# Kernel tuning notes

Measured on AMD Instinct MI355X. Metric: run time of the kernel, lower is better.

The kernel has to match this reference:

```python
import jax, jax.numpy as jnp
import numpy as np

H, D, BD = 4, 128, 128   # num_heads, head_dim, bias_dim
QDIM = KDIM = 64
VDIM = 1
N = 512
EPS = 1e-5

def mish(x):
    return x * jnp.tanh(jax.nn.softplus(x))

def layernorm(x, g, b):
    m = jnp.mean(x, axis=-1, keepdims=True)
    v = jnp.var(x, axis=-1, keepdims=True)
    return (x - m) * jax.lax.rsqrt(v + EPS) * g + b

def _xavier(k, shape):
    fan_out, fan_in = shape
    lim = np.sqrt(6.0 / (fan_in + fan_out)).astype(np.float32)
    return jax.random.uniform(k, shape, jnp.float32, -lim, lim)

def setup_inputs() -> dict:
    key = jax.random.key(0)
    ks = jax.random.split(key, 12)
    return {
        "q": jax.random.normal(ks[0], (N, QDIM), jnp.float32),
        "k": jax.random.normal(ks[1], (N, KDIM), jnp.float32),
        "v": jax.random.normal(ks[2], (N, VDIM), jnp.float32),
        "bias": jax.random.uniform(ks[3], (N, N, BD), jnp.float32),
        "Wq": _xavier(ks[4], (H * D, QDIM)), "bq": jnp.zeros((H * D,), jnp.float32),
        "Wk": _xavier(ks[5], (H * D, KDIM)), "bk": jnp.zeros((H * D,), jnp.float32),
        "Wqo": _xavier(ks[6], (QDIM, H * D)), "bqo": jnp.zeros((QDIM,), jnp.float32),
        "Wko": _xavier(ks[7], (KDIM, H * D)), "bko": jnp.zeros((KDIM,), jnp.float32),
        "q_ln_g": jnp.ones((QDIM,), jnp.float32), "q_ln_b": jnp.zeros((QDIM,), jnp.float32),
        "k_ln_g": jnp.ones((KDIM,), jnp.float32), "k_ln_b": jnp.zeros((KDIM,), jnp.float32),
        "Wb": _xavier(ks[8], (H * BD, BD)), "bb_": jnp.zeros((H * BD,), jnp.float32),
        "Wbo": _xavier(ks[9], (BD, H * BD)), "bbo": jnp.zeros((BD,), jnp.float32),
    }

def reference(q, k, v, bias, Wq, bq, Wk, bk, Wqo, bqo, Wko, bko,
              q_ln_g, q_ln_b, k_ln_g, k_ln_b, Wb, bb_, Wbo, bbo):
    Nq, Nk = q.shape[0], k.shape[0]
    # q/k projections -> [N, H, D]
    pq = (q @ Wq.T + bq).reshape(Nq, H, D)
    pk = (k @ Wk.T + bk).reshape(Nk, H, D)
    # distance bias: Linear(BD -> H*BD), per-head L2 norm -> [H, Nq, Nk]
    bias_p = bias @ Wb.T + bb_                                  # [Nq, Nk, H*BD]
    diffs = jnp.linalg.norm(bias_p.reshape(Nq, Nk, H, BD), axis=-1)  # [Nq, Nk, H]
    diffs = jnp.transpose(diffs, (2, 0, 1))                     # [H, Nq, Nk]
    # scaled dot product attention with additive distance bias
    logits = jnp.einsum('qhd,khd->hqk', pq, pk) / np.sqrt(D).astype(np.float32) + diffs
    attn = jax.nn.softmax(logits, axis=-1)                      # [H, Nq, Nk]
    vals = jnp.einsum('hqk,kv->hqv', attn, v)                   # v shared across heads
    # values.permute(1,0,2).reshape(Nq, vdim*H) then mean over last dim
    vals_mean = jnp.mean(jnp.transpose(vals, (1, 0, 2)).reshape(Nq, H * VDIM),
                         axis=-1, keepdims=True)                # [Nq, 1]
    # torch does proj.permute(1,2,0).reshape(N, H*D): (d, h)-major flattening
    pq_flat = jnp.transpose(pq, (0, 2, 1)).reshape(Nq, D * H)
    pk_flat = jnp.transpose(pk, (0, 2, 1)).reshape(Nk, D * H)
    q_new = layernorm(q + mish(pq_flat @ Wqo.T + bqo), q_ln_g, q_ln_b)
    k_new = layernorm(k + mish(pk_flat @ Wko.T + bko), k_ln_g, k_ln_b)
    bias_out = mish(bias_p @ Wbo.T + bbo)                       # [Nq, Nk, BD]
    return (q_new, k_new, vals_mean, bias_out)
```

## Files before the change

### kernel.cpp

```cpp
#include <hip/hip_runtime.h>

#define NN 512
#define MROWS (NN*NN)
#define LDK 136

typedef __attribute__((ext_vector_type(8))) short short8;
typedef __attribute__((ext_vector_type(16))) float floatx16;

__device__ __forceinline__ unsigned short f2bf(float f) {
    union { float f; unsigned u; } x; x.f = f;
    unsigned r = x.u + 0x7fffu + ((x.u >> 16) & 1u);
    return (unsigned short)(r >> 16);
}

__device__ __forceinline__ floatx16 zero16() {
    floatx16 z;
    #pragma unroll
    for (int i = 0; i < 16; ++i) z[i] = 0.f;
    return z;
}

__global__ __launch_bounds__(256) void pre_kernel(
    const float* __restrict__ q, const float* __restrict__ k,
    const float* __restrict__ Wq, const float* __restrict__ bq,
    const float* __restrict__ Wk, const float* __restrict__ bk,
    float* __restrict__ pq, float* __restrict__ pk,
    const float* __restrict__ Wb, const float* __restrict__ Wbo,
    unsigned short* __restrict__ wbf)
{
    int b = blockIdx.x;
    int tid = threadIdx.x;
    if (b >= 1024) {
        int i = (b - 1024) * 256 + tid;
        float v = (i < 65536) ? Wb[i] : Wbo[i - 65536];
        wbf[i] = f2bf(v);
        return;
    }
    __shared__ float xs[64];
    int n = b & 511;
    int is_k = b >> 9;
    const float* x  = is_k ? k  : q;
    const float* W  = is_k ? Wk : Wq;
    const float* bi = is_k ? bk : bq;
    float* out      = is_k ? pk : pq;
    if (tid < 16)
        reinterpret_cast<float4*>(xs)[tid] = reinterpret_cast<const float4*>(x + n*64)[tid];
    __syncthreads();
    #pragma unroll
    for (int jj = 0; jj < 2; ++jj) {
        int j = jj*256 + tid;
        const float4* wr = reinterpret_cast<const float4*>(W + j*64);
        float acc = bi[j];
        #pragma unroll
        for (int c = 0; c < 16; ++c) {
            float4 w4 = wr[c];
            float4 x4 = reinterpret_cast<const float4*>(xs)[c];
            acc += x4.x*w4.x + x4.y*w4.y + x4.z*w4.z + x4.w*w4.w;
        }
        out[n*512 + j] = acc;
    }
}

__global__ __launch_bounds__(256, 4) void bias_kernel(
    const float* __restrict__ bias, const unsigned short* __restrict__ wb_bf,
    const float* __restrict__ bb, const unsigned short* __restrict__ wbo_bf,
    const float* __restrict__ bbo, float* __restrict__ bias_out,
    float* __restrict__ diffs)
{
    __shared__ __align__(16) char smem[34816 + 256];
    unsigned short* lA = (unsigned short*)smem;
    unsigned short* lP = (unsigned short*)(smem + 17408);
    float* sq = (float*)(smem + 34816);
    float* lT = (float*)smem;

    const int tid = threadIdx.x;
    const int w   = tid >> 6;
    const int l   = tid & 63;
    const int l31 = l & 31;
    const int qh  = l >> 5;
    const long row0 = (long)blockIdx.x * 64;

    {
        const float* src = bias + row0 * 128;
        #pragma unroll
        for (int i = 0; i < 4; ++i) {
            int flat = i*2048 + tid*8;
            int r = flat >> 7, c = flat & 127;
            float4 v0 = *reinterpret_cast<const float4*>(src + flat);
            float4 v1 = *reinterpret_cast<const float4*>(src + flat + 4);
            ushort4 o0 = { f2bf(v0.x), f2bf(v0.y), f2bf(v0.z), f2bf(v0.w) };
            ushort4 o1 = { f2bf(v1.x), f2bf(v1.y), f2bf(v1.z), f2bf(v1.w) };
            *reinterpret_cast<ushort4*>(&lA[r*LDK + c])     = o0;
            *reinterpret_cast<ushort4*>(&lA[r*LDK + c + 4]) = o1;
        }
        if (tid < 64) sq[tid] = 0.f;
    }

    floatx16 acc2[2];
    acc2[0] = zero16(); acc2[1] = zero16();

    const unsigned short* wbbase  = wb_bf  + (w*32 + l31)*128 + qh*8;
    const unsigned short* wbobase = wbo_bf + (w*32 + l31)*512 + qh*8;

    __syncthreads();

    for (int h = 0; h < 4; ++h) {
        floatx16 acc1[2];
        acc1[0] = zero16(); acc1[1] = zero16();
        const unsigned short* wa = wbbase + h*16384;
        #pragma unroll
        for (int kk = 0; kk < 8; ++kk) {
            short8 afr = *reinterpret_cast<const short8*>(wa + kk*16);
            short8 b0  = *reinterpret_cast<const short8*>(&lA[(l31)*LDK      + kk*16 + qh*8]);
            short8 b1  = *reinterpret_cast<const short8*>(&lA[(32 + l31)*LDK + kk*16 + qh*8]);
            acc1[0] = __builtin_amdgcn_mfma_f32_32x32x16_bf16(afr, b0, acc1[0], 0, 0, 0);
            acc1[1] = __builtin_amdgcn_mfma_f32_32x32x16_bf16(afr, b1, acc1[1], 0, 0, 0);
        }

        float4 bbq[4];
        #pragma unroll
        for (int s = 0; s < 4; ++s)
            bbq[s] = *reinterpret_cast<const float4*>(bb + h*128 + w*32 + qh*4 + s*8);

        float ssum[2];
        ushort4 pk4[2][4];
        #pragma unroll
        for (int nt = 0; nt < 2; ++nt) {
            float sa = 0.f;
            #pragma unroll
            for (int s = 0; s < 4; ++s) {
                const float* bbp = (const float*)&bbq[s];
                float v0 = acc1[nt][s*4+0] + bbp[0];
                float v1 = acc1[nt][s*4+1] + bbp[1];
                float v2 = acc1[nt][s*4+2] + bbp[2];
                float v3 = acc1[nt][s*4+3] + bbp[3];
                sa += v0*v0 + v1*v1 + v2*v2 + v3*v3;
                pk4[nt][s] = (ushort4){ f2bf(v0), f2bf(v1), f2bf(v2), f2bf(v3) };
            }
            sa += __shfl_xor(sa, 32);
            ssum[nt] = sa;
        }

        __syncthreads();

        #pragma unroll
        for (int nt = 0; nt < 2; ++nt) {
            int m = nt*32 + l31;
            #pragma unroll
            for (int s = 0; s < 4; ++s)
                *reinterpret_cast<ushort4*>(&lP[m*LDK + w*32 + qh*4 + s*8]) = pk4[nt][s];
            if (l < 32) atomicAdd(&sq[m], ssum[nt]);
        }

        __syncthreads();

        if (tid < 64) {
            float s2 = sq[tid];
            diffs[(long)h*MROWS + row0 + tid] = sqrtf(s2);
            sq[tid] = 0.f;
        }

        const unsigned short* wo = wbobase + h*128;
        #pragma unroll
        for (int kk = 0; kk < 8; ++kk) {
            short8 afr = *reinterpret_cast<const short8*>(wo + kk*16);
            short8 b0  = *reinterpret_cast<const short8*>(&lP[(l31)*LDK      + kk*16 + qh*8]);
            short8 b1  = *reinterpret_cast<const short8*>(&lP[(32 + l31)*LDK + kk*16 + qh*8]);
            acc2[0] = __builtin_amdgcn_mfma_f32_32x32x16_bf16(afr, b0, acc2[0], 0, 0, 0);
            acc2[1] = __builtin_amdgcn_mfma_f32_32x32x16_bf16(afr, b1, acc2[1], 0, 0, 0);
        }
    }

    float4 bboq[4];
    #pragma unroll
    for (int s = 0; s < 4; ++s)
        bboq[s] = *reinterpret_cast<const float4*>(bbo + w*32 + qh*4 + s*8);

    float outs[2][16];
    #pragma unroll
    for (int nt = 0; nt < 2; ++nt) {
        #pragma unroll
        for (int s = 0; s < 4; ++s) {
            const float* bp = (const float*)&bboq[s];
            #pragma unroll
            for (int r = 0; r < 4; ++r) {
                float x = acc2[nt][s*4+r] + bp[r];
                float e = __expf(x);
                float u = 1.f + e, u2 = u*u;
                outs[nt][s*4+r] = (x > 15.f) ? x : x * (u2 - 1.f) / (u2 + 1.f);
            }
        }
    }

    __syncthreads();
    #pragma unroll
    for (int nt = 0; nt < 2; ++nt) {
        int m = nt*32 + l31;
        #pragma unroll
        for (int s = 0; s < 4; ++s)
            #pragma unroll
            for (int r = 0; r < 4; ++r)
                lT[m*LDK + w*32 + qh*4 + s*8 + r] = outs[nt][s*4+r];
    }
    __syncthreads();
    #pragma unroll
    for (int i = 0; i < 8; ++i) {
        int flat = i*1024 + tid*4;
        int r = flat >> 7, c = flat & 127;
        *reinterpret_cast<float4*>(bias_out + (row0 + r)*128 + c) =
            *reinterpret_cast<const float4*>(&lT[r*LDK + c]);
    }
}

__global__ __launch_bounds__(256) void qk_kernel(
    const float* __restrict__ pq, const float* __restrict__ pk,
    float* __restrict__ logits)
{
    __shared__ float A[64*128];
    __shared__ float BT[128*64];
    int blk = blockIdx.x;
    int kt = blk & 7, h = (blk >> 3) & 3, qt = blk >> 5;
    int tid = threadIdx.x;

    #pragma unroll
    for (int i = 0; i < 8; ++i) {
        int flat = i*1024 + tid*4;
        int r = flat >> 7, c = flat & 127;
        *reinterpret_cast<float4*>(&A[flat]) =
            *reinterpret_cast<const float4*>(pq + (size_t)(qt*64 + r)*512 + h*128 + c);
    }
    {
        int kk = tid & 63, g = tid >> 6;
        #pragma unroll
        for (int i = 0; i < 8; ++i) {
            int d0 = g*32 + i*4;
            float4 vv = *reinterpret_cast<const float4*>(pk + (size_t)(kt*64 + kk)*512 + h*128 + d0);
            BT[(d0+0)*64 + kk] = vv.x;
            BT[(d0+1)*64 + kk] = vv.y;
            BT[(d0+2)*64 + kk] = vv.z;
            BT[(d0+3)*64 + kk] = vv.w;
        }
    }
    __syncthreads();

    int qg = tid >> 4, kg = tid & 15;
    int qs = qg*4, ks = kg*4;
    float acc[4][4] = {};
    for (int d = 0; d < 128; d += 4) {
        float a_[4][4], b_[4][4];
        #pragma unroll
        for (int i = 0; i < 4; ++i) {
            float4 av = *reinterpret_cast<const float4*>(&A[(qs+i)*128 + d]);
            a_[i][0] = av.x; a_[i][1] = av.y; a_[i][2] = av.z; a_[i][3] = av.w;
        }
        #pragma unroll
        for (int dd = 0; dd < 4; ++dd) {
            float4 bv = *reinterpret_cast<const float4*>(&BT[(d+dd)*64 + ks]);
            b_[dd][0] = bv.x; b_[dd][1] = bv.y; b_[dd][2] = bv.z; b_[dd][3] = bv.w;
        }
        #pragma unroll
        for (int i = 0; i < 4; ++i)
            #pragma unroll
            for (int j = 0; j < 4; ++j)
                acc[i][j] += a_[i][0]*b_[0][j] + a_[i][1]*b_[1][j]
                           + a_[i][2]*b_[2][j] + a_[i][3]*b_[3][j];
    }

    const float scale = 0.088388347648318447f;
    #pragma unroll
    for (int i = 0; i < 4; ++i) {
        size_t off = (size_t)h*MROWS + (size_t)(qt*64 + qs + i)*512 + kt*64 + ks;
        float4* p = reinterpret_cast<float4*>(logits + off);
        float4 dv = *p;
        dv.x = fmaf(acc[i][0], scale, dv.x);
        dv.y = fmaf(acc[i][1], scale, dv.y);
        dv.z = fmaf(acc[i][2], scale, dv.z);
        dv.w = fmaf(acc[i][3], scale, dv.w);
        *p = dv;
    }
}

__global__ __launch_bounds__(256) void attnval_kernel(
    const float* __restrict__ logits, const float* __restrict__ v,
    float* __restrict__ vmean)
{
    __shared__ float red[32];
    int qrow = blockIdx.x, tid = threadIdx.x;
    int wid = tid >> 6;
    float vsum = 0.f;
    float v0 = v[tid], v1 = v[tid + 256];
    for (int h = 0; h < 4; ++h) {
        const float* lr = logits + (size_t)h*MROWS + (size_t)qrow*512;
        float l0 = lr[tid], l1 = lr[tid + 256];
        float m = fmaxf(l0, l1);
        #pragma unroll
        for (int o = 1; o < 64; o <<= 1) m = fmaxf(m, __shfl_xor(m, o));
        if ((tid & 63) == 0) red[wid] = m;
        __syncthreads();
        m = fmaxf(fmaxf(red[0], red[1]), fmaxf(red[2], red[3]));
        float e0 = __expf(l0 - m), e1 = __expf(l1 - m);
        float s = e0 + e1;
        float sv = e0*v0 + e1*v1;
        #pragma unroll
        for (int o = 1; o < 64; o <<= 1) { s += __shfl_xor(s, o); sv += __shfl_xor(sv, o); }
        __syncthreads();
        if ((tid & 63) == 0) { red[8 + wid] = s; red[16 + wid] = sv; }
        __syncthreads();
        float S  = red[8]  + red[9]  + red[10] + red[11];
        float SV = red[16] + red[17] + red[18] + red[19];
        vsum += SV / S;
        __syncthreads();
    }
    if (tid == 0) vmean[qrow] = vsum * 0.25f;
}

__global__ __launch_bounds__(256) void qkout_kernel(
    const float* __restrict__ p, const float* __restrict__ x,
    const float* __restrict__ W, const float* __restrict__ bo,
    const float* __restrict__ g, const float* __restrict__ be,
    float* __restrict__ out)
{
    __shared__ float pr[512];
    __shared__ float red[256];
    int n = blockIdx.x, tid = threadIdx.x;
    if (tid < 128)
        reinterpret_cast<float4*>(pr)[tid] = reinterpret_cast<const float4*>(p + (size_t)n*512)[tid];
    __syncthreads();
    int o = tid >> 2, part = tid & 3;
    const float4* wr = reinterpret_cast<const float4*>(W + o*512 + part*128);
    float acc = 0.f;
    #pragma unroll
    for (int c = 0; c < 32; ++c) {
        float4 w4 = wr[c];
        int base = part*32 + c;
        acc += pr[base]*w4.x + pr[128 + base]*w4.y + pr[256 + base]*w4.z + pr[384 + base]*w4.w;
    }
    red[tid] = acc;
    __syncthreads();
    if (tid < 64) {
        float s = red[tid*4] + red[tid*4+1] + red[tid*4+2] + red[tid*4+3] + bo[tid];
        float e = __expf(s);
        float u = 1.f + e, u2 = u*u;
        float msh = (s > 15.f) ? s : s * (u2 - 1.f) / (u2 + 1.f);
        float val = x[n*64 + tid] + msh;
        float m = val, m2 = val*val;
        #pragma unroll
        for (int off = 1; off < 64; off <<= 1) { m += __shfl_xor(m, off); m2 += __shfl_xor(m2, off); }
        m *= (1.f/64.f); m2 *= (1.f/64.f);
        float var = m2 - m*m;
        out[n*64 + tid] = (val - m) * rsqrtf(var + 1e-5f) * g[tid] + be[tid];
    }
}

extern "C" void kernel_launch(void* const* d_in, const int* in_sizes, int n_in,
                              void* d_out, int out_size, void* d_ws, size_t ws_size,
                              hipStream_t stream) {
    const float* q    = (const float*)d_in[0];
    const float* k    = (const float*)d_in[1];
    const float* v    = (const float*)d_in[2];
    const float* bias = (const float*)d_in[3];
    const float* Wq   = (const float*)d_in[4];
    const float* bq   = (const float*)d_in[5];
    const float* Wk   = (const float*)d_in[6];
    const float* bk   = (const float*)d_in[7];
    const float* Wqo  = (const float*)d_in[8];
    const float* bqo  = (const float*)d_in[9];
    const float* Wko  = (const float*)d_in[10];
    const float* bko  = (const float*)d_in[11];
    const float* qlg  = (const float*)d_in[12];
    const float* qlb  = (const float*)d_in[13];
    const float* klg  = (const float*)d_in[14];
    const float* klb  = (const float*)d_in[15];
    const float* Wb   = (const float*)d_in[16];
    const float* bb   = (const float*)d_in[17];
    const float* Wbo  = (const float*)d_in[18];
    const float* bbo  = (const float*)d_in[19];

    float* out = (float*)d_out;
    float* ws  = (float*)d_ws;
    float* diffs = ws;
    float* pq    = ws + 4*MROWS;
    float* pk    = pq + MROWS;
    unsigned short* wbf = (unsigned short*)(pk + MROWS);

    float* q_new = out;
    float* k_new = out + 32768;
    float* vmean = out + 65536;
    float* b_out = out + 66048;

    pre_kernel<<<dim3(1536), dim3(256), 0, stream>>>(q, k, Wq, bq, Wk, bk, pq, pk, Wb, Wbo, wbf);
    bias_kernel<<<dim3(4096), dim3(256), 0, stream>>>(bias, wbf, bb, wbf + 65536, bbo, b_out, diffs);
    qk_kernel<<<dim3(256), dim3(256), 0, stream>>>(pq, pk, diffs);
    attnval_kernel<<<dim3(512), dim3(256), 0, stream>>>(diffs, v, vmean);
    qkout_kernel<<<dim3(512), dim3(256), 0, stream>>>(pq, q, Wqo, bqo, qlg, qlb, q_new);
    qkout_kernel<<<dim3(512), dim3(256), 0, stream>>>(pk, k, Wko, bko, klg, klb, k_new);
}
```

Measured before the change: 444.1 us.

## Keep bias MLP tiles in registers per wave, dropping LDS and block barriers

Restructures the fused bias kernel so that each wave owns 32 rows and computes every output column itself. The bias fragments stay in registers, the intermediate projection is reshuffled into MFMA B-fragments with lane shuffles, and results are written straight to global memory. This removes the LDS staging, the atomic norm reduction and several __syncthreads per head. In exchange, weight fragments are reloaded from global or L2 by every wave, register pressure rises (launch bounds drop to 2 waves per SIMD), and output stores are less coalesced.

```diff
diff --git a/kernel.cpp b/kernel.cpp
--- a/kernel.cpp
+++ b/kernel.cpp
@@ -2,7 +2,6 @@
 
 #define NN 512
 #define MROWS (NN*NN)
-#define LDK 136
 
 typedef __attribute__((ext_vector_type(8))) short short8;
 typedef __attribute__((ext_vector_type(16))) float floatx16;
@@ -11,6 +10,10 @@
     union { float f; unsigned u; } x; x.f = f;
     unsigned r = x.u + 0x7fffu + ((x.u >> 16) & 1u);
     return (unsigned short)(r >> 16);
+}
+
+__device__ __forceinline__ unsigned pack2bf(float a, float b) {
+    return (unsigned)f2bf(a) | ((unsigned)f2bf(b) << 16);
 }
 
 __device__ __forceinline__ floatx16 zero16() {
@@ -61,154 +64,114 @@
     }
 }
 
-__global__ __launch_bounds__(256, 4) void bias_kernel(
+__global__ __launch_bounds__(256, 2) void bias_kernel(
     const float* __restrict__ bias, const unsigned short* __restrict__ wb_bf,
     const float* __restrict__ bb, const unsigned short* __restrict__ wbo_bf,
     const float* __restrict__ bbo, float* __restrict__ bias_out,
     float* __restrict__ diffs)
 {
-    __shared__ __align__(16) char smem[34816 + 256];
-    unsigned short* lA = (unsigned short*)smem;
-    unsigned short* lP = (unsigned short*)(smem + 17408);
-    float* sq = (float*)(smem + 34816);
-    float* lT = (float*)smem;
-
     const int tid = threadIdx.x;
     const int w   = tid >> 6;
     const int l   = tid & 63;
     const int l31 = l & 31;
     const int qh  = l >> 5;
-    const long row0 = (long)blockIdx.x * 64;
-
+    const long row = (long)blockIdx.x * 128 + w*32 + l31;
+
+    short8 bias_fr[8];
     {
-        const float* src = bias + row0 * 128;
-        #pragma unroll
-        for (int i = 0; i < 4; ++i) {
-            int flat = i*2048 + tid*8;
-            int r = flat >> 7, c = flat & 127;
-            float4 v0 = *reinterpret_cast<const float4*>(src + flat);
-            float4 v1 = *reinterpret_cast<const float4*>(src + flat + 4);
-            ushort4 o0 = { f2bf(v0.x), f2bf(v0.y), f2bf(v0.z), f2bf(v0.w) };
-            ushort4 o1 = { f2bf(v1.x), f2bf(v1.y), f2bf(v1.z), f2bf(v1.w) };
-            *reinterpret_cast<ushort4*>(&lA[r*LDK + c])     = o0;
-            *reinterpret_cast<ushort4*>(&lA[r*LDK + c + 4]) = o1;
-        }
-        if (tid < 64) sq[tid] = 0.f;
-    }
-
-    floatx16 acc2[2];
-    acc2[0] = zero16(); acc2[1] = zero16();
-
-    const unsigned short* wbbase  = wb_bf  + (w*32 + l31)*128 + qh*8;
-    const unsigned short* wbobase = wbo_bf + (w*32 + l31)*512 + qh*8;
-
-    __syncthreads();
+        const float* brow = bias + row*128 + qh*8;
+        #pragma unroll
+        for (int kk = 0; kk < 8; ++kk) {
+            float4 v0 = *reinterpret_cast<const float4*>(brow + kk*16);
+            float4 v1 = *reinterpret_cast<const float4*>(brow + kk*16 + 4);
+            short8 t;
+            t[0] = (short)f2bf(v0.x); t[1] = (short)f2bf(v0.y);
+            t[2] = (short)f2bf(v0.z); t[3] = (short)f2bf(v0.w);
+            t[4] = (short)f2bf(v1.x); t[5] = (short)f2bf(v1.y);
+            t[6] = (short)f2bf(v1.z); t[7] = (short)f2bf(v1.w);
+            bias_fr[kk] = t;
+        }
+    }
+
+    floatx16 acc2[4];
+    acc2[0] = zero16(); acc2[1] = zero16(); acc2[2] = zero16(); acc2[3] = zero16();
+
+    const unsigned short* wbbase  = wb_bf  + l31*128 + qh*8;
+    const unsigned short* wbobase = wbo_bf + l31*512 + qh*8;
 
     for (int h = 0; h < 4; ++h) {
-        floatx16 acc1[2];
-        acc1[0] = zero16(); acc1[1] = zero16();
-        const unsigned short* wa = wbbase + h*16384;
+        floatx16 acc1[4];
+        acc1[0] = zero16(); acc1[1] = zero16(); acc1[2] = zero16(); acc1[3] = zero16();
+        const unsigned short* wh = wbbase + h*16384;
         #pragma unroll
         for (int kk = 0; kk < 8; ++kk) {
-            short8 afr = *reinterpret_cast<const short8*>(wa + kk*16);
-            short8 b0  = *reinterpret_cast<const short8*>(&lA[(l31)*LDK      + kk*16 + qh*8]);
-            short8 b1  = *reinterpret_cast<const short8*>(&lA[(32 + l31)*LDK + kk*16 + qh*8]);
-            acc1[0] = __builtin_amdgcn_mfma_f32_32x32x16_bf16(afr, b0, acc1[0], 0, 0, 0);
-            acc1[1] = __builtin_amdgcn_mfma_f32_32x32x16_bf16(afr, b1, acc1[1], 0, 0, 0);
-        }
-
-        float4 bbq[4];
-        #pragma unroll
-        for (int s = 0; s < 4; ++s)
-            bbq[s] = *reinterpret_cast<const float4*>(bb + h*128 + w*32 + qh*4 + s*8);
-
-        float ssum[2];
-        ushort4 pk4[2][4];
-        #pragma unroll
-        for (int nt = 0; nt < 2; ++nt) {
-            float sa = 0.f;
-            #pragma unroll
-            for (int s = 0; s < 4; ++s) {
-                const float* bbp = (const float*)&bbq[s];
-                float v0 = acc1[nt][s*4+0] + bbp[0];
-                float v1 = acc1[nt][s*4+1] + bbp[1];
-                float v2 = acc1[nt][s*4+2] + bbp[2];
-                float v3 = acc1[nt][s*4+3] + bbp[3];
-                sa += v0*v0 + v1*v1 + v2*v2 + v3*v3;
-                pk4[nt][s] = (ushort4){ f2bf(v0), f2bf(v1), f2bf(v2), f2bf(v3) };
+            #pragma unroll
+            for (int nt = 0; nt < 4; ++nt) {
+                short8 afr = *reinterpret_cast<const short8*>(wh + nt*4096 + kk*16);
+                acc1[nt] = __builtin_amdgcn_mfma_f32_32x32x16_bf16(afr, bias_fr[kk], acc1[nt], 0, 0, 0);
             }
-            sa += __shfl_xor(sa, 32);
-            ssum[nt] = sa;
-        }
-
-        __syncthreads();
-
-        #pragma unroll
-        for (int nt = 0; nt < 2; ++nt) {
-            int m = nt*32 + l31;
-            #pragma unroll
-            for (int s = 0; s < 4; ++s)
-                *reinterpret_cast<ushort4*>(&lP[m*LDK + w*32 + qh*4 + s*8]) = pk4[nt][s];
-            if (l < 32) atomicAdd(&sq[m], ssum[nt]);
-        }
-
-        __syncthreads();
-
-        if (tid < 64) {
-            float s2 = sq[tid];
-            diffs[(long)h*MROWS + row0 + tid] = sqrtf(s2);
-            sq[tid] = 0.f;
-        }
+        }
+
+        float ssq = 0.f;
+        short8 bfr[8];
+        #pragma unroll
+        for (int kk2 = 0; kk2 < 8; ++kk2) {
+            const int nt = kk2 >> 1, s0 = (kk2 & 1) * 2;
+            unsigned a0, b0, a1, b1;
+            #pragma unroll
+            for (int si = 0; si < 2; ++si) {
+                const int s = s0 + si;
+                float4 bb4 = *reinterpret_cast<const float4*>(bb + h*128 + nt*32 + s*8 + qh*4);
+                float v0 = acc1[nt][s*4+0] + bb4.x;
+                float v1 = acc1[nt][s*4+1] + bb4.y;
+                float v2 = acc1[nt][s*4+2] + bb4.z;
+                float v3 = acc1[nt][s*4+3] + bb4.w;
+                ssq += v0*v0 + v1*v1 + v2*v2 + v3*v3;
+                unsigned pa = pack2bf(v0, v1);
+                unsigned pb = pack2bf(v2, v3);
+                if (si == 0) { a0 = pa; b0 = pb; } else { a1 = pa; b1 = pb; }
+            }
+            unsigned sa0 = __shfl_xor(a0, 32), sb0 = __shfl_xor(b0, 32);
+            unsigned sa1 = __shfl_xor(a1, 32), sb1 = __shfl_xor(b1, 32);
+            union { unsigned u[4]; short8 v; } cv;
+            cv.u[0] = qh ? sa1 : a0;
+            cv.u[1] = qh ? sb1 : b0;
+            cv.u[2] = qh ? a1  : sa0;
+            cv.u[3] = qh ? b1  : sb0;
+            bfr[kk2] = cv.v;
+        }
+        ssq += __shfl_xor(ssq, 32);
+        if (l < 32) diffs[(long)h*MROWS + row] = sqrtf(ssq);
 
         const unsigned short* wo = wbobase + h*128;
         #pragma unroll
-        for (int kk = 0; kk < 8; ++kk) {
-            short8 afr = *reinterpret_cast<const short8*>(wo + kk*16);
-            short8 b0  = *reinterpret_cast<const short8*>(&lP[(l31)*LDK      + kk*16 + qh*8]);
-            short8 b1  = *reinterpret_cast<const short8*>(&lP[(32 + l31)*LDK + kk*16 + qh*8]);
-            acc2[0] = __builtin_amdgcn_mfma_f32_32x32x16_bf16(afr, b0, acc2[0], 0, 0, 0);
-            acc2[1] = __builtin_amdgcn_mfma_f32_32x32x16_bf16(afr, b1, acc2[1], 0, 0, 0);
-        }
-    }
-
-    float4 bboq[4];
-    #pragma unroll
-    for (int s = 0; s < 4; ++s)
-        bboq[s] = *reinterpret_cast<const float4*>(bbo + w*32 + qh*4 + s*8);
-
-    float outs[2][16];
-    #pragma unroll
-    for (int nt = 0; nt < 2; ++nt) {
+        for (int kk2 = 0; kk2 < 8; ++kk2) {
+            #pragma unroll
+            for (int nt2 = 0; nt2 < 4; ++nt2) {
+                short8 afr = *reinterpret_cast<const short8*>(wo + nt2*16384 + kk2*16);
+                acc2[nt2] = __builtin_amdgcn_mfma_f32_32x32x16_bf16(afr, bfr[kk2], acc2[nt2], 0, 0, 0);
+            }
+        }
+    }
+
+    float* orow = bias_out + row*128;
+    #pragma unroll
+    for (int nt2 = 0; nt2 < 4; ++nt2) {
         #pragma unroll
         for (int s = 0; s < 4; ++s) {
-            const float* bp = (const float*)&bboq[s];
+            float4 bo4 = *reinterpret_cast<const float4*>(bbo + nt2*32 + s*8 + qh*4);
+            const float* bp = (const float*)&bo4;
+            float o[4];
             #pragma unroll
             for (int r = 0; r < 4; ++r) {
-                float x = acc2[nt][s*4+r] + bp[r];
+                float x = acc2[nt2][s*4+r] + bp[r];
                 float e = __expf(x);
                 float u = 1.f + e, u2 = u*u;
-                outs[nt][s*4+r] = (x > 15.f) ? x : x * (u2 - 1.f) / (u2 + 1.f);
+                o[r] = (x > 15.f) ? x : x * (u2 - 1.f) / (u2 + 1.f);
             }
-        }
-    }
-
-    __syncthreads();
-    #pragma unroll
-    for (int nt = 0; nt < 2; ++nt) {
-        int m = nt*32 + l31;
-        #pragma unroll
-        for (int s = 0; s < 4; ++s)
-            #pragma unroll
-            for (int r = 0; r < 4; ++r)
-                lT[m*LDK + w*32 + qh*4 + s*8 + r] = outs[nt][s*4+r];
-    }
-    __syncthreads();
-    #pragma unroll
-    for (int i = 0; i < 8; ++i) {
-        int flat = i*1024 + tid*4;
-        int r = flat >> 7, c = flat & 127;
-        *reinterpret_cast<float4*>(bias_out + (row0 + r)*128 + c) =
-            *reinterpret_cast<const float4*>(&lT[r*LDK + c]);
+            float4 ov = { o[0], o[1], o[2], o[3] };
+            *reinterpret_cast<float4*>(orow + nt2*32 + s*8 + qh*4) = ov;
+        }
     }
 }
 
@@ -389,7 +352,7 @@
     float* b_out = out + 66048;
 
     pre_kernel<<<dim3(1536), dim3(256), 0, stream>>>(q, k, Wq, bq, Wk, bk, pq, pk, Wb, Wbo, wbf);
-    bias_kernel<<<dim3(4096), dim3(256), 0, stream>>>(bias, wbf, bb, wbf + 65536, bbo, b_out, diffs);
+    bias_kernel<<<dim3(2048), dim3(256), 0, stream>>>(bias, wbf, bb, wbf + 65536, bbo, b_out, diffs);
     qk_kernel<<<dim3(256), dim3(256), 0, stream>>>(pq, pk, diffs);
     attnval_kernel<<<dim3(512), dim3(256), 0, stream>>>(diffs, v, vmean);
     qkout_kernel<<<dim3(512), dim3(256), 0, stream>>>(pq, q, Wqo, bqo, qlg, qlb, q_new);
```

Result: slower. 586.4 us (+32.1%).

## Halve bias_kernel LDS staging buffers to raise occupancy to six blocks

Applied to the files above, without the earlier changes.

Shrinks the bias kernel's shared memory by staging the bf16 intermediate and the fp32 output tile in two halves instead of whole. The second-GEMM K loop and the output write-back are split into two phases with extra barriers. The launch bound goes from 4 to 6 blocks per CU. The aim is more waves in flight to hide memory latency on this bandwidth-heavy kernel, at the cost of extra synchronisation and a tighter register budget.

```diff
diff --git a/kernel.cpp b/kernel.cpp
--- a/kernel.cpp
+++ b/kernel.cpp
@@ -3,6 +3,7 @@
 #define NN 512
 #define MROWS (NN*NN)
 #define LDK 136
+#define LDP 72
 
 typedef __attribute__((ext_vector_type(8))) short short8;
 typedef __attribute__((ext_vector_type(16))) float floatx16;
@@ -61,17 +62,17 @@
     }
 }
 
-__global__ __launch_bounds__(256, 4) void bias_kernel(
+__global__ __launch_bounds__(256, 6) void bias_kernel(
     const float* __restrict__ bias, const unsigned short* __restrict__ wb_bf,
     const float* __restrict__ bb, const unsigned short* __restrict__ wbo_bf,
     const float* __restrict__ bbo, float* __restrict__ bias_out,
     float* __restrict__ diffs)
 {
-    __shared__ __align__(16) char smem[34816 + 256];
-    unsigned short* lA = (unsigned short*)smem;
-    unsigned short* lP = (unsigned short*)(smem + 17408);
-    float* sq = (float*)(smem + 34816);
-    float* lT = (float*)smem;
+    __shared__ __align__(16) char smem[26880];
+    unsigned short* lA  = (unsigned short*)smem;
+    unsigned short* lPh = (unsigned short*)(smem + 17408);
+    float* sq = (float*)(smem + 26624);
+    float* lTh = (float*)smem;
 
     const int tid = threadIdx.x;
     const int w   = tid >> 6;
@@ -146,10 +147,16 @@
         #pragma unroll
         for (int nt = 0; nt < 2; ++nt) {
             int m = nt*32 + l31;
-            #pragma unroll
-            for (int s = 0; s < 4; ++s)
-                *reinterpret_cast<ushort4*>(&lP[m*LDK + w*32 + qh*4 + s*8]) = pk4[nt][s];
             if (l < 32) atomicAdd(&sq[m], ssum[nt]);
+        }
+        if (w < 2) {
+            #pragma unroll
+            for (int nt = 0; nt < 2; ++nt) {
+                int m = nt*32 + l31;
+                #pragma unroll
+                for (int s = 0; s < 4; ++s)
+                    *reinterpret_cast<ushort4*>(&lPh[m*LDP + (w&1)*32 + qh*4 + s*8]) = pk4[nt][s];
+            }
         }
 
         __syncthreads();
@@ -162,10 +169,33 @@
 
         const unsigned short* wo = wbobase + h*128;
         #pragma unroll
-        for (int kk = 0; kk < 8; ++kk) {
-            short8 afr = *reinterpret_cast<const short8*>(wo + kk*16);
-            short8 b0  = *reinterpret_cast<const short8*>(&lP[(l31)*LDK      + kk*16 + qh*8]);
-            short8 b1  = *reinterpret_cast<const short8*>(&lP[(32 + l31)*LDK + kk*16 + qh*8]);
+        for (int kkl = 0; kkl < 4; ++kkl) {
+            short8 afr = *reinterpret_cast<const short8*>(wo + kkl*16);
+            short8 b0  = *reinterpret_cast<const short8*>(&lPh[(l31)*LDP      + kkl*16 + qh*8]);
+            short8 b1  = *reinterpret_cast<const short8*>(&lPh[(32 + l31)*LDP + kkl*16 + qh*8]);
+            acc2[0] = __builtin_amdgcn_mfma_f32_32x32x16_bf16(afr, b0, acc2[0], 0, 0, 0);
+            acc2[1] = __builtin_amdgcn_mfma_f32_32x32x16_bf16(afr, b1, acc2[1], 0, 0, 0);
+        }
+
+        __syncthreads();
+
+        if (w >= 2) {
+            #pragma unroll
+            for (int nt = 0; nt < 2; ++nt) {
+                int m = nt*32 + l31;
+                #pragma unroll
+                for (int s = 0; s < 4; ++s)
+                    *reinterpret_cast<ushort4*>(&lPh[m*LDP + (w&1)*32 + qh*4 + s*8]) = pk4[nt][s];
+            }
+        }
+
+        __syncthreads();
+
+        #pragma unroll
+        for (int kkl = 0; kkl < 4; ++kkl) {
+            short8 afr = *reinterpret_cast<const short8*>(wo + (4 + kkl)*16);
+            short8 b0  = *reinterpret_cast<const short8*>(&lPh[(l31)*LDP      + kkl*16 + qh*8]);
+            short8 b1  = *reinterpret_cast<const short8*>(&lPh[(32 + l31)*LDP + kkl*16 + qh*8]);
             acc2[0] = __builtin_amdgcn_mfma_f32_32x32x16_bf16(afr, b0, acc2[0], 0, 0, 0);
             acc2[1] = __builtin_amdgcn_mfma_f32_32x32x16_bf16(afr, b1, acc2[1], 0, 0, 0);
         }
@@ -194,21 +224,27 @@
 
     __syncthreads();
     #pragma unroll
-    for (int nt = 0; nt < 2; ++nt) {
-        int m = nt*32 + l31;
-        #pragma unroll
-        for (int s = 0; s < 4; ++s)
-            #pragma unroll
-            for (int r = 0; r < 4; ++r)
-                lT[m*LDK + w*32 + qh*4 + s*8 + r] = outs[nt][s*4+r];
-    }
-    __syncthreads();
-    #pragma unroll
-    for (int i = 0; i < 8; ++i) {
-        int flat = i*1024 + tid*4;
-        int r = flat >> 7, c = flat & 127;
-        *reinterpret_cast<float4*>(bias_out + (row0 + r)*128 + c) =
-            *reinterpret_cast<const float4*>(&lT[r*LDK + c]);
+    for (int half = 0; half < 2; ++half) {
+        if ((w >> 1) == half) {
+            #pragma unroll
+            for (int nt = 0; nt < 2; ++nt) {
+                int m = nt*32 + l31;
+                #pragma unroll
+                for (int s = 0; s < 4; ++s)
+                    #pragma unroll
+                    for (int r = 0; r < 4; ++r)
+                        lTh[m*68 + (w&1)*32 + s*8 + qh*4 + r] = outs[nt][s*4+r];
+            }
+        }
+        __syncthreads();
+        #pragma unroll
+        for (int i = 0; i < 4; ++i) {
+            int flat = i*1024 + tid*4;
+            int r = flat >> 6, c = flat & 63;
+            *reinterpret_cast<float4*>(bias_out + (row0 + r)*128 + half*64 + c) =
+                *reinterpret_cast<const float4*>(&lTh[r*68 + c]);
+        }
+        __syncthreads();
     }
 }
 
```

Result: slower. 532.6 us (+19.9%).

## Fuse QK logits into attention kernel and split bias kernel across 8 waves

Applied to the files above, without the earlier changes.

Removes the separate qk_kernel and computes the scaled q·k dot products inside attnval_kernel, reading diffs directly and dropping the read-modify-write of the logits buffer. The bias kernel moves to 512 threads per block, with each wave handling one 32-row half of the 64-row tile instead of both, which halves the per-wave MFMA chain and accumulator registers. The fused attention recomputes the dot products per query row using uncoalesced strided pk loads from global memory, and the larger block may reduce occupancy.

```diff
diff --git a/kernel.cpp b/kernel.cpp
--- a/kernel.cpp
+++ b/kernel.cpp
@@ -61,7 +61,7 @@
     }
 }
 
-__global__ __launch_bounds__(256, 4) void bias_kernel(
+__global__ __launch_bounds__(512, 6) void bias_kernel(
     const float* __restrict__ bias, const unsigned short* __restrict__ wb_bf,
     const float* __restrict__ bb, const unsigned short* __restrict__ wbo_bf,
     const float* __restrict__ bbo, float* __restrict__ bias_out,
@@ -75,16 +75,19 @@
 
     const int tid = threadIdx.x;
     const int w   = tid >> 6;
+    const int nsl = w & 3;
+    const int mh  = w >> 2;
     const int l   = tid & 63;
     const int l31 = l & 31;
     const int qh  = l >> 5;
     const long row0 = (long)blockIdx.x * 64;
+    const int m = mh*32 + l31;
 
     {
         const float* src = bias + row0 * 128;
         #pragma unroll
-        for (int i = 0; i < 4; ++i) {
-            int flat = i*2048 + tid*8;
+        for (int i = 0; i < 2; ++i) {
+            int flat = i*4096 + tid*8;
             int r = flat >> 7, c = flat & 127;
             float4 v0 = *reinterpret_cast<const float4*>(src + flat);
             float4 v1 = *reinterpret_cast<const float4*>(src + flat + 4);
@@ -96,61 +99,43 @@
         if (tid < 64) sq[tid] = 0.f;
     }
 
-    floatx16 acc2[2];
-    acc2[0] = zero16(); acc2[1] = zero16();
-
-    const unsigned short* wbbase  = wb_bf  + (w*32 + l31)*128 + qh*8;
-    const unsigned short* wbobase = wbo_bf + (w*32 + l31)*512 + qh*8;
+    floatx16 acc2 = zero16();
+
+    const unsigned short* wbbase  = wb_bf  + (nsl*32 + l31)*128 + qh*8;
+    const unsigned short* wbobase = wbo_bf + (nsl*32 + l31)*512 + qh*8;
 
     __syncthreads();
 
     for (int h = 0; h < 4; ++h) {
-        floatx16 acc1[2];
-        acc1[0] = zero16(); acc1[1] = zero16();
+        floatx16 acc1 = zero16();
         const unsigned short* wa = wbbase + h*16384;
         #pragma unroll
         for (int kk = 0; kk < 8; ++kk) {
             short8 afr = *reinterpret_cast<const short8*>(wa + kk*16);
-            short8 b0  = *reinterpret_cast<const short8*>(&lA[(l31)*LDK      + kk*16 + qh*8]);
-            short8 b1  = *reinterpret_cast<const short8*>(&lA[(32 + l31)*LDK + kk*16 + qh*8]);
-            acc1[0] = __builtin_amdgcn_mfma_f32_32x32x16_bf16(afr, b0, acc1[0], 0, 0, 0);
-            acc1[1] = __builtin_amdgcn_mfma_f32_32x32x16_bf16(afr, b1, acc1[1], 0, 0, 0);
-        }
-
-        float4 bbq[4];
+            short8 bf  = *reinterpret_cast<const short8*>(&lA[m*LDK + kk*16 + qh*8]);
+            acc1 = __builtin_amdgcn_mfma_f32_32x32x16_bf16(afr, bf, acc1, 0, 0, 0);
+        }
+
+        float sa = 0.f;
+        ushort4 pk4[4];
+        #pragma unroll
+        for (int s = 0; s < 4; ++s) {
+            float4 bb4 = *reinterpret_cast<const float4*>(bb + h*128 + nsl*32 + s*8 + qh*4);
+            float v0 = acc1[s*4+0] + bb4.x;
+            float v1 = acc1[s*4+1] + bb4.y;
+            float v2 = acc1[s*4+2] + bb4.z;
+            float v3 = acc1[s*4+3] + bb4.w;
+            sa += v0*v0 + v1*v1 + v2*v2 + v3*v3;
+            pk4[s] = (ushort4){ f2bf(v0), f2bf(v1), f2bf(v2), f2bf(v3) };
+        }
+        sa += __shfl_xor(sa, 32);
+
+        __syncthreads();
+
         #pragma unroll
         for (int s = 0; s < 4; ++s)
-            bbq[s] = *reinterpret_cast<const float4*>(bb + h*128 + w*32 + qh*4 + s*8);
-
-        float ssum[2];
-        ushort4 pk4[2][4];
-        #pragma unroll
-        for (int nt = 0; nt < 2; ++nt) {
-            float sa = 0.f;
-            #pragma unroll
-            for (int s = 0; s < 4; ++s) {
-                const float* bbp = (const float*)&bbq[s];
-                float v0 = acc1[nt][s*4+0] + bbp[0];
-                float v1 = acc1[nt][s*4+1] + bbp[1];
-                float v2 = acc1[nt][s*4+2] + bbp[2];
-                float v3 = acc1[nt][s*4+3] + bbp[3];
-                sa += v0*v0 + v1*v1 + v2*v2 + v3*v3;
-                pk4[nt][s] = (ushort4){ f2bf(v0), f2bf(v1), f2bf(v2), f2bf(v3) };
-            }
-            sa += __shfl_xor(sa, 32);
-            ssum[nt] = sa;
-        }
-
-        __syncthreads();
-
-        #pragma unroll
-        for (int nt = 0; nt < 2; ++nt) {
-            int m = nt*32 + l31;
-            #pragma unroll
-            for (int s = 0; s < 4; ++s)
-                *reinterpret_cast<ushort4*>(&lP[m*LDK + w*32 + qh*4 + s*8]) = pk4[nt][s];
-            if (l < 32) atomicAdd(&sq[m], ssum[nt]);
-        }
+            *reinterpret_cast<ushort4*>(&lP[m*LDK + nsl*32 + qh*4 + s*8]) = pk4[s];
+        if (l < 32) atomicAdd(&sq[m], sa);
 
         __syncthreads();
 
@@ -164,134 +149,72 @@
         #pragma unroll
         for (int kk = 0; kk < 8; ++kk) {
             short8 afr = *reinterpret_cast<const short8*>(wo + kk*16);
-            short8 b0  = *reinterpret_cast<const short8*>(&lP[(l31)*LDK      + kk*16 + qh*8]);
-            short8 b1  = *reinterpret_cast<const short8*>(&lP[(32 + l31)*LDK + kk*16 + qh*8]);
-            acc2[0] = __builtin_amdgcn_mfma_f32_32x32x16_bf16(afr, b0, acc2[0], 0, 0, 0);
-            acc2[1] = __builtin_amdgcn_mfma_f32_32x32x16_bf16(afr, b1, acc2[1], 0, 0, 0);
-        }
-    }
-
-    float4 bboq[4];
+            short8 bf  = *reinterpret_cast<const short8*>(&lP[m*LDK + kk*16 + qh*8]);
+            acc2 = __builtin_amdgcn_mfma_f32_32x32x16_bf16(afr, bf, acc2, 0, 0, 0);
+        }
+    }
+
+    float outs[16];
+    #pragma unroll
+    for (int s = 0; s < 4; ++s) {
+        float4 bo4 = *reinterpret_cast<const float4*>(bbo + nsl*32 + s*8 + qh*4);
+        const float* bp = (const float*)&bo4;
+        #pragma unroll
+        for (int r = 0; r < 4; ++r) {
+            float x = acc2[s*4+r] + bp[r];
+            float e = __expf(x);
+            float u = 1.f + e, u2 = u*u;
+            outs[s*4+r] = (x > 15.f) ? x : x * (u2 - 1.f) / (u2 + 1.f);
+        }
+    }
+
+    __syncthreads();
     #pragma unroll
     for (int s = 0; s < 4; ++s)
-        bboq[s] = *reinterpret_cast<const float4*>(bbo + w*32 + qh*4 + s*8);
-
-    float outs[2][16];
-    #pragma unroll
-    for (int nt = 0; nt < 2; ++nt) {
-        #pragma unroll
-        for (int s = 0; s < 4; ++s) {
-            const float* bp = (const float*)&bboq[s];
-            #pragma unroll
-            for (int r = 0; r < 4; ++r) {
-                float x = acc2[nt][s*4+r] + bp[r];
-                float e = __expf(x);
-                float u = 1.f + e, u2 = u*u;
-                outs[nt][s*4+r] = (x > 15.f) ? x : x * (u2 - 1.f) / (u2 + 1.f);
-            }
-        }
-    }
-
-    __syncthreads();
-    #pragma unroll
-    for (int nt = 0; nt < 2; ++nt) {
-        int m = nt*32 + l31;
-        #pragma unroll
-        for (int s = 0; s < 4; ++s)
-            #pragma unroll
-            for (int r = 0; r < 4; ++r)
-                lT[m*LDK + w*32 + qh*4 + s*8 + r] = outs[nt][s*4+r];
-    }
-    __syncthreads();
-    #pragma unroll
-    for (int i = 0; i < 8; ++i) {
-        int flat = i*1024 + tid*4;
+        #pragma unroll
+        for (int r = 0; r < 4; ++r)
+            lT[m*136 + nsl*32 + s*8 + qh*4 + r] = outs[s*4+r];
+    __syncthreads();
+    #pragma unroll
+    for (int i = 0; i < 4; ++i) {
+        int flat = i*2048 + tid*4;
         int r = flat >> 7, c = flat & 127;
         *reinterpret_cast<float4*>(bias_out + (row0 + r)*128 + c) =
-            *reinterpret_cast<const float4*>(&lT[r*LDK + c]);
-    }
-}
-
-__global__ __launch_bounds__(256) void qk_kernel(
-    const float* __restrict__ pq, const float* __restrict__ pk,
-    float* __restrict__ logits)
-{
-    __shared__ float A[64*128];
-    __shared__ float BT[128*64];
-    int blk = blockIdx.x;
-    int kt = blk & 7, h = (blk >> 3) & 3, qt = blk >> 5;
-    int tid = threadIdx.x;
-
-    #pragma unroll
-    for (int i = 0; i < 8; ++i) {
-        int flat = i*1024 + tid*4;
-        int r = flat >> 7, c = flat & 127;
-        *reinterpret_cast<float4*>(&A[flat]) =
-            *reinterpret_cast<const float4*>(pq + (size_t)(qt*64 + r)*512 + h*128 + c);
-    }
-    {
-        int kk = tid & 63, g = tid >> 6;
-        #pragma unroll
-        for (int i = 0; i < 8; ++i) {
-            int d0 = g*32 + i*4;
-            float4 vv = *reinterpret_cast<const float4*>(pk + (size_t)(kt*64 + kk)*512 + h*128 + d0);
-            BT[(d0+0)*64 + kk] = vv.x;
-            BT[(d0+1)*64 + kk] = vv.y;
-            BT[(d0+2)*64 + kk] = vv.z;
-            BT[(d0+3)*64 + kk] = vv.w;
-        }
-    }
-    __syncthreads();
-
-    int qg = tid >> 4, kg = tid & 15;
-    int qs = qg*4, ks = kg*4;
-    float acc[4][4] = {};
-    for (int d = 0; d < 128; d += 4) {
-        float a_[4][4], b_[4][4];
-        #pragma unroll
-        for (int i = 0; i < 4; ++i) {
-            float4 av = *reinterpret_cast<const float4*>(&A[(qs+i)*128 + d]);
-            a_[i][0] = av.x; a_[i][1] = av.y; a_[i][2] = av.z; a_[i][3] = av.w;
-        }
-        #pragma unroll
-        for (int dd = 0; dd < 4; ++dd) {
-            float4 bv = *reinterpret_cast<const float4*>(&BT[(d+dd)*64 + ks]);
-            b_[dd][0] = bv.x; b_[dd][1] = bv.y; b_[dd][2] = bv.z; b_[dd][3] = bv.w;
-        }
-        #pragma unroll
-        for (int i = 0; i < 4; ++i)
-            #pragma unroll
-            for (int j = 0; j < 4; ++j)
-                acc[i][j] += a_[i][0]*b_[0][j] + a_[i][1]*b_[1][j]
-                           + a_[i][2]*b_[2][j] + a_[i][3]*b_[3][j];
-    }
-
-    const float scale = 0.088388347648318447f;
-    #pragma unroll
-    for (int i = 0; i < 4; ++i) {
-        size_t off = (size_t)h*MROWS + (size_t)(qt*64 + qs + i)*512 + kt*64 + ks;
-        float4* p = reinterpret_cast<float4*>(logits + off);
-        float4 dv = *p;
-        dv.x = fmaf(acc[i][0], scale, dv.x);
-        dv.y = fmaf(acc[i][1], scale, dv.y);
-        dv.z = fmaf(acc[i][2], scale, dv.z);
-        dv.w = fmaf(acc[i][3], scale, dv.w);
-        *p = dv;
+            *reinterpret_cast<const float4*>(&lT[r*136 + c]);
     }
 }
 
 __global__ __launch_bounds__(256) void attnval_kernel(
-    const float* __restrict__ logits, const float* __restrict__ v,
+    const float* __restrict__ diffs, const float* __restrict__ pq,
+    const float* __restrict__ pk, const float* __restrict__ v,
     float* __restrict__ vmean)
 {
+    __shared__ float qs[512];
     __shared__ float red[32];
     int qrow = blockIdx.x, tid = threadIdx.x;
     int wid = tid >> 6;
+    if (tid < 128)
+        reinterpret_cast<float4*>(qs)[tid] = reinterpret_cast<const float4*>(pq + (size_t)qrow*512)[tid];
+    __syncthreads();
+    float v0 = v[tid], v1 = v[tid + 256];
     float vsum = 0.f;
-    float v0 = v[tid], v1 = v[tid + 256];
+    const float scale = 0.088388347648318447f;
     for (int h = 0; h < 4; ++h) {
-        const float* lr = logits + (size_t)h*MROWS + (size_t)qrow*512;
-        float l0 = lr[tid], l1 = lr[tid + 256];
+        const float* dr = diffs + (size_t)h*MROWS + (size_t)qrow*512;
+        const float4* qh4 = reinterpret_cast<const float4*>(qs + h*128);
+        const float4* pk0 = reinterpret_cast<const float4*>(pk + (size_t)tid*512 + h*128);
+        const float4* pk1 = reinterpret_cast<const float4*>(pk + (size_t)(tid+256)*512 + h*128);
+        float acc0 = 0.f, acc1 = 0.f;
+        #pragma unroll
+        for (int c = 0; c < 32; ++c) {
+            float4 a  = qh4[c];
+            float4 b0 = pk0[c];
+            float4 b1 = pk1[c];
+            acc0 += a.x*b0.x + a.y*b0.y + a.z*b0.z + a.w*b0.w;
+            acc1 += a.x*b1.x + a.y*b1.y + a.z*b1.z + a.w*b1.w;
+        }
+        float l0 = fmaf(acc0, scale, dr[tid]);
+        float l1 = fmaf(acc1, scale, dr[tid + 256]);
         float m = fmaxf(l0, l1);
         #pragma unroll
         for (int o = 1; o < 64; o <<= 1) m = fmaxf(m, __shfl_xor(m, o));
@@ -389,9 +312,8 @@
     float* b_out = out + 66048;
 
     pre_kernel<<<dim3(1536), dim3(256), 0, stream>>>(q, k, Wq, bq, Wk, bk, pq, pk, Wb, Wbo, wbf);
-    bias_kernel<<<dim3(4096), dim3(256), 0, stream>>>(bias, wbf, bb, wbf + 65536, bbo, b_out, diffs);
-    qk_kernel<<<dim3(256), dim3(256), 0, stream>>>(pq, pk, diffs);
-    attnval_kernel<<<dim3(512), dim3(256), 0, stream>>>(diffs, v, vmean);
+    bias_kernel<<<dim3(4096), dim3(512), 0, stream>>>(bias, wbf, bb, wbf + 65536, bbo, b_out, diffs);
+    attnval_kernel<<<dim3(512), dim3(256), 0, stream>>>(diffs, pq, pk, v, vmean);
     qkout_kernel<<<dim3(512), dim3(256), 0, stream>>>(pq, q, Wqo, bqo, qlg, qlb, q_new);
     qkout_kernel<<<dim3(512), dim3(256), 0, stream>>>(pk, k, Wko, bko, klg, klb, k_new);
 }
```

Result: slower. 627.4 us (+41.3%).
